# Optimization experiments

Measured on AMD Instinct MI355X. Metric: run time of the kernel, lower is better.

## Reference

```python
import jax, jax.numpy as jnp
import numpy as np

TREND_SCALING = 0.6
DETAIL_PRESERVATION = 0.85
SPIKE_THRESHOLD = 3.5
SPIKE_DAMPING = 0.35
ITERATIONS = 2
BASE_WINDOW = 5
STRIDE = max(1, BASE_WINDOW // 2)  # 2
R = BASE_WINDOW                    # 5
EPS = 1e-6


def setup_inputs() -> dict:
    key = jax.random.key(0)
    B, C, L = 4, 4, 1048576
    x = jax.random.normal(key, (B, C, L), dtype=jnp.float32)
    # registered buffers: normalized box kernels (1/window)
    detail_kernel = jnp.ones((1, 1, BASE_WINDOW), jnp.float32) / float(BASE_WINDOW)
    trend_kernel = jnp.ones((1, 1, BASE_WINDOW * 2 + 1), jnp.float32) / float(BASE_WINDOW * 2 + 1)
    return {"x": x, "detail_kernel": detail_kernel, "trend_kernel": trend_kernel}


def _smooth(x, kernel):
    # depthwise (grouped) conv1d with reflect padding, same length out
    pad = kernel.shape[-1] // 2
    xp = jnp.pad(x, ((0, 0), (0, 0), (pad, pad)), mode="reflect")
    C = x.shape[1]
    w = jnp.broadcast_to(kernel, (C, 1, kernel.shape[-1]))
    return jax.lax.conv_general_dilated(
        xp, w, window_strides=(1,), padding="VALID",
        dimension_numbers=("NCH", "OIH", "NCH"), feature_group_count=C)


def _denoise_pass(x, detail_kernel, trend_kernel):
    B, C, L = x.shape
    trend = _smooth(x, trend_kernel)
    local = _smooth(x, detail_kernel)
    residual = x - local
    # torch .std() is unbiased (ddof=1)
    scale = jnp.maximum(jnp.std(residual, axis=-1, keepdims=True, ddof=1), EPS)
    threshold = scale * SPIKE_THRESHOLD
    residual = jnp.where(jnp.abs(residual) > threshold, residual * SPIKE_DAMPING, residual)
    residual = residual * DETAIL_PRESERVATION
    blended = (1.0 - TREND_SCALING) * local + TREND_SCALING * trend
    xp = blended + residual

    remainder = (L - R) % STRIDE
    pad_right = 0 if remainder == 0 else STRIDE - remainder
    if pad_right > 0:
        xp = jnp.pad(xp, ((0, 0), (0, 0), (0, pad_right)), mode="reflect")
    L_pad = xp.shape[-1]

    # overlap-add scatter-mean (faithful to torch unfold + scatter_add_ + count)
    n_ranges = (L_pad - R) // STRIDE + 1
    starts = jnp.arange(n_ranges) * STRIDE                      # [N]
    idx = (starts[:, None] + jnp.arange(R)[None, :]).reshape(-1)  # [N*R]
    xf = xp.reshape(B * C, L_pad)
    segments = xf[:, idx]                                       # [BC, N*R] unfold windows
    out = jnp.zeros((B * C, L_pad), xf.dtype).at[:, idx].add(segments)
    count = jnp.zeros((L_pad,), xf.dtype).at[idx].add(1.0)
    out = out / jnp.maximum(count, 1.0)[None, :]
    return out.reshape(B, C, L_pad)[:, :, :L]


def reference(x, detail_kernel, trend_kernel):
    cur = x.astype(jnp.float32)
    for _ in range(ITERATIONS):
        cur = _denoise_pass(cur, detail_kernel, trend_kernel)
    return cur.astype(x.dtype)
```

## Files before the change

### kernel.cpp

```cpp
#include <hip/hip_runtime.h>

#define NTHREADS 256
#define EPT      8
#define CHUNK    (NTHREADS*EPT)
#define ROWS     16
#define NB       2048
#define BPR      (NB/ROWS)
#define CPB      4

#define C_TREND   0.6f
#define C_DETAIL  0.85f
#define C_SPIKE_T 3.5f
#define C_SPIKE_D 0.35f
#define C_EPS     1e-6f
#define B5   0.08f
#define B11  0.05454545454545454f

#define SKEW(m) ((m) + ((m) >> 3))

typedef float vfloat4 __attribute__((ext_vector_type(4)));

__device__ __forceinline__ float reflect_load(const float* __restrict__ rp, int g, int L) {
    if (g < 0) g = -g;
    else if (g >= L) g = 2 * L - 2 - g;
    return rp[g];
}

__device__ __forceinline__ void blk_reduce2(double& s, double& s2) {
    #pragma unroll
    for (int off = 32; off > 0; off >>= 1) {
        s  += __shfl_xor(s, off);
        s2 += __shfl_xor(s2, off);
    }
    __shared__ double lds[8];
    int wid = threadIdx.x >> 6, lane = threadIdx.x & 63;
    if (lane == 0) { lds[2*wid] = s; lds[2*wid+1] = s2; }
    __syncthreads();
    s  = lds[0] + lds[2] + lds[4] + lds[6];
    s2 = lds[1] + lds[3] + lds[5] + lds[7];
}

__device__ __forceinline__ float var_to_thr(double s, double s2, int L) {
    double n = (double)L;
    double var = (s2 - s * s / n) / (n - 1.0);
    float stdv = (float)sqrt(fmax(var, 0.0));
    return fmaxf(stdv, C_EPS) * C_SPIKE_T;
}

__device__ __forceinline__ float thr128(const double* __restrict__ prow, int L) {
    __shared__ float thr_s;
    if (threadIdx.x < 64) {
        int l = threadIdx.x;
        double s  = prow[2*l + 0] + prow[2*(l+64) + 0];
        double s2 = prow[2*l + 1] + prow[2*(l+64) + 1];
        #pragma unroll
        for (int off = 32; off > 0; off >>= 1) {
            s  += __shfl_xor(s, off);
            s2 += __shfl_xor(s2, off);
        }
        if (threadIdx.x == 0) thr_s = var_to_thr(s, s2, L);
    }
    __syncthreads();
    return thr_s;
}

__device__ float xp1_scalar(const float* __restrict__ rp, int L, int p, float thr) {
    if (p < 0) p = -p;
    else if (p >= L) p = 2 * L - 2 - p;
    float s5 = 0.f, s11 = 0.f;
    #pragma unroll
    for (int k = -5; k <= 5; ++k) {
        float v = reflect_load(rp, p + k, L);
        s11 += v;
        if (k >= -2 && k <= 2) s5 += v;
    }
    float r = fmaf(-0.2f, s5, rp[p]);
    r = (fabsf(r) > thr) ? r * C_SPIKE_D : r;
    return fmaf(C_DETAIL, r, fmaf(B11, s11, B5 * s5));
}

__device__ __forceinline__ void load_w24(const float* __restrict__ rp, int o, int L, float w[24]) {
    if (o >= 8 && o + 16 <= L) {
        const float4* p = reinterpret_cast<const float4*>(rp + o - 8);
        #pragma unroll
        for (int j = 0; j < 6; ++j) {
            float4 v = p[j];
            w[4*j+0] = v.x; w[4*j+1] = v.y; w[4*j+2] = v.z; w[4*j+3] = v.w;
        }
    } else {
        #pragma unroll
        for (int j = 0; j < 24; ++j) w[j] = reflect_load(rp, o - 8 + j, L);
    }
}

__device__ __forceinline__ void xp1_slide8(const float w[24], float t1, float pv[8]) {
    float s5  = w[6] + w[7] + w[8] + w[9] + w[10];
    float s11 = w[3] + w[4] + w[5] + w[6] + w[7] + w[8]
              + w[9] + w[10] + w[11] + w[12] + w[13];
    #pragma unroll
    for (int k = 0; k < 8; ++k) {
        float r = fmaf(-0.2f, s5, w[8 + k]);
        r = (fabsf(r) > t1) ? r * C_SPIKE_D : r;
        pv[k] = fmaf(C_DETAIL, r, fmaf(B11, s11, B5 * s5));
        if (k < 7) { s5 += w[11 + k] - w[6 + k]; s11 += w[14 + k] - w[3 + k]; }
    }
}

__global__ __launch_bounds__(NTHREADS) void k1_reduce(
    const float* __restrict__ x, double* __restrict__ partials1, int L) {
    int row = blockIdx.x / BPR, cgid = blockIdx.x % BPR;
    const float* rp = x + (size_t)row * L;
    double s = 0.0, s2 = 0.0;
    for (int i = 0; i < CPB; ++i) {
        int o = (cgid * CPB + i) * CHUNK + threadIdx.x * EPT;
        float w[16];
        if (o >= 4 && o + 12 <= L) {
            const float4* p = reinterpret_cast<const float4*>(rp + o - 4);
            #pragma unroll
            for (int j = 0; j < 4; ++j) {
                float4 v = p[j];
                w[4*j+0] = v.x; w[4*j+1] = v.y; w[4*j+2] = v.z; w[4*j+3] = v.w;
            }
        } else {
            #pragma unroll
            for (int j = 0; j < 16; ++j) w[j] = reflect_load(rp, o - 4 + j, L);
        }
        float s5 = w[2] + w[3] + w[4] + w[5] + w[6];
        #pragma unroll
        for (int k = 0; k < EPT; ++k) {
            float r = fmaf(-0.2f, s5, w[4 + k]);
            s += (double)r;
            s2 = fma((double)r, (double)r, s2);
            if (k < EPT - 1) s5 += w[7 + k] - w[2 + k];
        }
    }
    blk_reduce2(s, s2);
    if (threadIdx.x == 0) { partials1[2*blockIdx.x] = s; partials1[2*blockIdx.x+1] = s2; }
}

__global__ __launch_bounds__(NTHREADS) void k2_reduce(
    const float* __restrict__ x, const double* __restrict__ partials1,
    double* __restrict__ partials2, int L) {
    __shared__ float xpbuf[2][SKEW(CHUNK + 4 - 1) + 1];
    int row = blockIdx.x / BPR, cgid = blockIdx.x % BPR;
    const float* rp = x + (size_t)row * L;
    float t1 = thr128(partials1 + (size_t)row * 2 * BPR, L);
    int tid = threadIdx.x;
    double s = 0.0, s2 = 0.0;
    for (int i = 0; i < CPB; ++i) {
        float* xp = xpbuf[i & 1];
        int cb = (cgid * CPB + i) * CHUNK;
        int o = cb + tid * EPT;
        float w[24];
        load_w24(rp, o, L, w);
        float pv[8];
        xp1_slide8(w, t1, pv);
        int m2b = tid * EPT + 2;
        #pragma unroll
        for (int k = 0; k < 8; ++k) xp[SKEW(m2b + k)] = pv[k];
        if (tid < 2)                     xp[SKEW(tid)] = xp1_scalar(rp, L, cb - 2 + tid, t1);
        else if (tid >= 64 && tid < 66)  xp[SKEW(CHUNK + 2 + (tid-64))] = xp1_scalar(rp, L, cb + CHUNK + (tid-64), t1);
        __syncthreads();
        float v2[12];
        v2[0] = xp[SKEW(m2b - 2)];
        v2[1] = xp[SKEW(m2b - 1)];
        #pragma unroll
        for (int k = 0; k < 8; ++k) v2[2+k] = pv[k];
        v2[10] = xp[SKEW(m2b + 8)];
        v2[11] = xp[SKEW(m2b + 9)];
        float t5 = v2[0]+v2[1]+v2[2]+v2[3]+v2[4];
        #pragma unroll
        for (int k = 0; k < EPT; ++k) {
            float r2 = fmaf(-0.2f, t5, v2[2+k]);
            s += (double)r2;
            s2 = fma((double)r2, (double)r2, s2);
            if (k < EPT - 1) t5 += v2[5+k] - v2[k];
        }
    }
    blk_reduce2(s, s2);
    if (threadIdx.x == 0) { partials2[2*blockIdx.x] = s; partials2[2*blockIdx.x+1] = s2; }
}

__global__ __launch_bounds__(NTHREADS) void k3_apply(
    const float* __restrict__ x, const double* __restrict__ partials1,
    const double* __restrict__ partials2, float* __restrict__ out, int L) {
    __shared__ float xpbuf[2][SKEW(CHUNK + 10 - 1) + 1];
    int row = blockIdx.x / BPR, cgid = blockIdx.x % BPR;
    const float* rp = x + (size_t)row * L;
    float* orow = out + (size_t)row * L;
    float t1 = thr128(partials1 + (size_t)row * 2 * BPR, L);
    float t2 = thr128(partials2 + (size_t)row * 2 * BPR, L);
    int tid = threadIdx.x;
    for (int i = 0; i < CPB; ++i) {
        float* xp = xpbuf[i & 1];
        int cb = (cgid * CPB + i) * CHUNK;
        int o = cb + tid * EPT;
        float w[24];
        load_w24(rp, o, L, w);
        float pv[8];
        xp1_slide8(w, t1, pv);
        int m2b = tid * EPT + 5;
        #pragma unroll
        for (int k = 0; k < 8; ++k) xp[SKEW(m2b + k)] = pv[k];
        if (tid < 5)                     xp[SKEW(tid)] = xp1_scalar(rp, L, cb - 5 + tid, t1);
        else if (tid >= 64 && tid < 69)  xp[SKEW(CHUNK + 5 + (tid-64))] = xp1_scalar(rp, L, cb + CHUNK + (tid-64), t1);
        __syncthreads();
        float w2[18];
        #pragma unroll
        for (int j = 0; j < 5; ++j) w2[j]    = xp[SKEW(m2b - 5 + j)];
        #pragma unroll
        for (int k = 0; k < 8; ++k) w2[5+k]  = pv[k];
        #pragma unroll
        for (int j = 0; j < 5; ++j) w2[13+j] = xp[SKEW(m2b + 8 + j)];
        float res[EPT];
        {
            float s5  = w2[3]+w2[4]+w2[5]+w2[6]+w2[7];
            float s11 = w2[0]+w2[1]+w2[2]+w2[3]+w2[4]+w2[5]
                      + w2[6]+w2[7]+w2[8]+w2[9]+w2[10];
            #pragma unroll
            for (int k = 0; k < EPT; ++k) {
                float r = fmaf(-0.2f, s5, w2[5+k]);
                r = (fabsf(r) > t2) ? r * C_SPIKE_D : r;
                res[k] = fmaf(C_DETAIL, r, fmaf(B11, s11, B5 * s5));
                if (k < EPT - 1) { s5 += w2[8+k] - w2[3+k]; s11 += w2[11+k] - w2[k]; }
            }
        }
        vfloat4 r0 = { res[0], res[1], res[2], res[3] };
        vfloat4 r1 = { res[4], res[5], res[6], res[7] };
        __builtin_nontemporal_store(r0, reinterpret_cast<vfloat4*>(orow + o));
        __builtin_nontemporal_store(r1, reinterpret_cast<vfloat4*>(orow + o) + 1);
    }
}

extern "C" void kernel_launch(void* const* d_in, const int* in_sizes, int n_in,
                              void* d_out, int out_size, void* d_ws, size_t ws_size,
                              hipStream_t stream) {
    const float* x = (const float*)d_in[0];
    float* outp = (float*)d_out;

    int total = in_sizes[0];
    int L = total / ROWS;

    double* partials1 = (double*)d_ws;
    double* partials2 = partials1 + 2 * NB;

    k1_reduce<<<NB, NTHREADS, 0, stream>>>(x, partials1, L);
    k2_reduce<<<NB, NTHREADS, 0, stream>>>(x, partials1, partials2, L);
    k3_apply <<<NB, NTHREADS, 0, stream>>>(x, partials1, partials2, outp, L);
}
```

Measured before the change: 57.57 us.

## Exchange stage-one halos via wavefront shuffles instead of shared memory

In the second-pass reduction and apply kernels, the neighbouring first-pass values each thread needs now come from adjacent lanes through shuffle-up/down. This replaces the shared-memory staging buffer and its block-wide barrier. Lanes at wavefront edges (0 and 63) compute their halo values directly from global memory using scalar recomputation, with a batched 5-element helper added for the apply kernel. That recomputation is extra redundant work done by divergent lanes in every wavefront, where before only a few lanes per block did it.

```diff
diff --git a/kernel.cpp b/kernel.cpp
--- a/kernel.cpp
+++ b/kernel.cpp
@@ -15,8 +15,6 @@
 #define C_EPS     1e-6f
 #define B5   0.08f
 #define B11  0.05454545454545454f
-
-#define SKEW(m) ((m) + ((m) >> 3))
 
 typedef float vfloat4 __attribute__((ext_vector_type(4)));
 
@@ -77,6 +75,27 @@
     float r = fmaf(-0.2f, s5, rp[p]);
     r = (fabsf(r) > thr) ? r * C_SPIKE_D : r;
     return fmaf(C_DETAIL, r, fmaf(B11, s11, B5 * s5));
+}
+
+__device__ __forceinline__ void xp1_scalar5(const float* __restrict__ rp, int L,
+                                            int base, float thr, float out[5]) {
+    if (base >= 0 && base + 4 < L) {
+        float w[15];
+        #pragma unroll
+        for (int j = 0; j < 15; ++j) w[j] = reflect_load(rp, base - 5 + j, L);
+        float s5  = w[3]+w[4]+w[5]+w[6]+w[7];
+        float s11 = w[0]+w[1]+w[2]+w[3]+w[4]+w[5]+w[6]+w[7]+w[8]+w[9]+w[10];
+        #pragma unroll
+        for (int k = 0; k < 5; ++k) {
+            float r = fmaf(-0.2f, s5, w[5+k]);
+            r = (fabsf(r) > thr) ? r * C_SPIKE_D : r;
+            out[k] = fmaf(C_DETAIL, r, fmaf(B11, s11, B5 * s5));
+            if (k < 4) { s5 += w[8+k] - w[3+k]; s11 += w[11+k] - w[k]; }
+        }
+    } else {
+        #pragma unroll
+        for (int k = 0; k < 5; ++k) out[k] = xp1_scalar(rp, L, base + k, thr);
+    }
 }
 
 __device__ __forceinline__ void load_w24(const float* __restrict__ rp, int o, int L, float w[24]) {
@@ -141,33 +160,33 @@
 __global__ __launch_bounds__(NTHREADS) void k2_reduce(
     const float* __restrict__ x, const double* __restrict__ partials1,
     double* __restrict__ partials2, int L) {
-    __shared__ float xpbuf[2][SKEW(CHUNK + 4 - 1) + 1];
     int row = blockIdx.x / BPR, cgid = blockIdx.x % BPR;
     const float* rp = x + (size_t)row * L;
     float t1 = thr128(partials1 + (size_t)row * 2 * BPR, L);
-    int tid = threadIdx.x;
+    int tid = threadIdx.x, lane = tid & 63;
     double s = 0.0, s2 = 0.0;
     for (int i = 0; i < CPB; ++i) {
-        float* xp = xpbuf[i & 1];
-        int cb = (cgid * CPB + i) * CHUNK;
-        int o = cb + tid * EPT;
+        int o = (cgid * CPB + i) * CHUNK + tid * EPT;
         float w[24];
         load_w24(rp, o, L, w);
         float pv[8];
         xp1_slide8(w, t1, pv);
-        int m2b = tid * EPT + 2;
-        #pragma unroll
-        for (int k = 0; k < 8; ++k) xp[SKEW(m2b + k)] = pv[k];
-        if (tid < 2)                     xp[SKEW(tid)] = xp1_scalar(rp, L, cb - 2 + tid, t1);
-        else if (tid >= 64 && tid < 66)  xp[SKEW(CHUNK + 2 + (tid-64))] = xp1_scalar(rp, L, cb + CHUNK + (tid-64), t1);
-        __syncthreads();
+        float hl0 = __shfl_up(pv[6], 1);
+        float hl1 = __shfl_up(pv[7], 1);
+        float hr0 = __shfl_down(pv[0], 1);
+        float hr1 = __shfl_down(pv[1], 1);
+        if (lane == 0) {
+            hl0 = xp1_scalar(rp, L, o - 2, t1);
+            hl1 = xp1_scalar(rp, L, o - 1, t1);
+        } else if (lane == 63) {
+            hr0 = xp1_scalar(rp, L, o + 8, t1);
+            hr1 = xp1_scalar(rp, L, o + 9, t1);
+        }
         float v2[12];
-        v2[0] = xp[SKEW(m2b - 2)];
-        v2[1] = xp[SKEW(m2b - 1)];
+        v2[0] = hl0; v2[1] = hl1;
         #pragma unroll
         for (int k = 0; k < 8; ++k) v2[2+k] = pv[k];
-        v2[10] = xp[SKEW(m2b + 8)];
-        v2[11] = xp[SKEW(m2b + 9)];
+        v2[10] = hr0; v2[11] = hr1;
         float t5 = v2[0]+v2[1]+v2[2]+v2[3]+v2[4];
         #pragma unroll
         for (int k = 0; k < EPT; ++k) {
@@ -184,34 +203,39 @@
 __global__ __launch_bounds__(NTHREADS) void k3_apply(
     const float* __restrict__ x, const double* __restrict__ partials1,
     const double* __restrict__ partials2, float* __restrict__ out, int L) {
-    __shared__ float xpbuf[2][SKEW(CHUNK + 10 - 1) + 1];
     int row = blockIdx.x / BPR, cgid = blockIdx.x % BPR;
     const float* rp = x + (size_t)row * L;
     float* orow = out + (size_t)row * L;
     float t1 = thr128(partials1 + (size_t)row * 2 * BPR, L);
     float t2 = thr128(partials2 + (size_t)row * 2 * BPR, L);
-    int tid = threadIdx.x;
+    int tid = threadIdx.x, lane = tid & 63;
     for (int i = 0; i < CPB; ++i) {
-        float* xp = xpbuf[i & 1];
-        int cb = (cgid * CPB + i) * CHUNK;
-        int o = cb + tid * EPT;
+        int o = (cgid * CPB + i) * CHUNK + tid * EPT;
         float w[24];
         load_w24(rp, o, L, w);
         float pv[8];
         xp1_slide8(w, t1, pv);
-        int m2b = tid * EPT + 5;
-        #pragma unroll
-        for (int k = 0; k < 8; ++k) xp[SKEW(m2b + k)] = pv[k];
-        if (tid < 5)                     xp[SKEW(tid)] = xp1_scalar(rp, L, cb - 5 + tid, t1);
-        else if (tid >= 64 && tid < 69)  xp[SKEW(CHUNK + 5 + (tid-64))] = xp1_scalar(rp, L, cb + CHUNK + (tid-64), t1);
-        __syncthreads();
+        float hl[5], hr[5];
+        #pragma unroll
+        for (int j = 0; j < 5; ++j) hl[j] = __shfl_up(pv[3 + j], 1);
+        #pragma unroll
+        for (int j = 0; j < 5; ++j) hr[j] = __shfl_down(pv[j], 1);
+        if (lane == 0) {
+            float edge[5];
+            xp1_scalar5(rp, L, o - 5, t1, edge);
+            for (int j = 0; j < 5; ++j) hl[j] = edge[j];
+        } else if (lane == 63) {
+            float edge[5];
+            xp1_scalar5(rp, L, o + 8, t1, edge);
+            for (int j = 0; j < 5; ++j) hr[j] = edge[j];
+        }
         float w2[18];
         #pragma unroll
-        for (int j = 0; j < 5; ++j) w2[j]    = xp[SKEW(m2b - 5 + j)];
+        for (int j = 0; j < 5; ++j) w2[j]    = hl[j];
         #pragma unroll
         for (int k = 0; k < 8; ++k) w2[5+k]  = pv[k];
         #pragma unroll
-        for (int j = 0; j < 5; ++j) w2[13+j] = xp[SKEW(m2b + 8 + j)];
+        for (int j = 0; j < 5; ++j) w2[13+j] = hr[j];
         float res[EPT];
         {
             float s5  = w2[3]+w2[4]+w2[5]+w2[6]+w2[7];
```

New measurement: 82.36 us. +43.1%, slower.
